# Performance work log

Hardware: AMD Instinct MI355X
Metric: run time of the kernel (lower is better)

## Reference

```python
import jax, jax.numpy as jnp
import numpy as np

LMAX_IN = 3
LMAX_OUT = 3
C = 64          # num_channel
H = 64          # num_channel_hidden
N_NODES = 2048
N_EDGES = 8192

# All coupled (l1, l2, l3) paths with |l1-l2| <= l3 <= min(l1+l2, lmax_out)
COMBS = [(l1, l2, l3)
         for l1 in range(LMAX_IN + 1)
         for l2 in range(LMAX_OUT + 1)
         for l3 in range(abs(l1 - l2), min(l1 + l2, LMAX_OUT) + 1)]
COUNTS = {l3: sum(1 for c in COMBS if c[2] == l3) for l3 in range(LMAX_OUT + 1)}

# Fixed coupling (Clebsch-Gordan-like) tensors for each path, shape (2l1+1, 2l2+1, 2l3+1).
# Deterministic constants (not trained / not differentiated), standing in for the
# e3nn CG coefficients used by InterEinsumTC.
_rng = np.random.RandomState(1234)
CG = [jnp.asarray((_rng.randn(2 * l1 + 1, 2 * l2 + 1, 2 * l3 + 1) * 0.2).astype(np.float32))
      for (l1, l2, l3) in COMBS]


def setup_inputs() -> dict:
    key = jax.random.key(0)
    ks = jax.random.split(key, 16)
    inp = {}
    for l in range(LMAX_OUT + 1):
        inp[f"x{l}"] = jax.random.normal(ks[l], (N_NODES, C, 2 * l + 1), dtype=jnp.float32)
        inp[f"y{l}"] = jax.random.normal(ks[4 + l], (N_EDGES, 2 * l + 1), dtype=jnp.float32)
        fan_in = C * COUNTS[l]
        inp[f"w_lin{l}"] = jax.random.normal(ks[8 + l], (fan_in, H), dtype=jnp.float32) / np.float32(np.sqrt(fan_in))
    inp["ws"] = jax.random.normal(ks[12], (N_EDGES, C * len(COMBS)), dtype=jnp.float32)
    inp["edge_index"] = jax.random.randint(ks[13], (2, N_EDGES), 0, N_NODES, dtype=jnp.int32)
    return inp


def _forward(x0, x1, x2, x3, y0, y1, y2, y3, ws, w_lin0, w_lin1, w_lin2, w_lin3, edge_index):
    xs = (x0, x1, x2, x3)
    ys = (y0, y1, y2, y3)
    wl = (w_lin0, w_lin1, w_lin2, w_lin3)
    src, dst = edge_index[0], edge_index[1]
    # per-edge gather of node features for every input degree
    xg = [x[src] for x in xs]                      # [E, C, 2l1+1]
    buf = {l3: [] for l3 in range(LMAX_OUT + 1)}
    for i, (l1, l2, l3) in enumerate(COMBS):
        # tensor-product contraction: [E, C, 2l3+1]
        out = jnp.einsum('lmn,ecl,em->ecn', CG[i], xg[l1], ys[l2])
        w = ws[:, i * C:(i + 1) * C][:, :, None]   # [E, C, 1] per-path per-channel weight
        buf[l3].append(w * out)
    res = []
    for l3 in range(LMAX_OUT + 1):
        m_ji = jnp.concatenate(buf[l3], axis=1)    # [E, C*count_l3, 2l3+1]
        m_i = jax.ops.segment_sum(m_ji, dst, num_segments=N_NODES)  # scatter-sum -> [N, C*count, 2l3+1]
        res.append(jnp.einsum('ncm,ch->nhm', m_i, wl[l3]))          # per-l3 linear -> [N, H, 2l3+1]
    return tuple(res)


def reference(x0, x1, x2, x3, y0, y1, y2, y3, ws, w_lin0, w_lin1, w_lin2, w_lin3, edge_index):
    return _forward(x0, x1, x2, x3, y0, y1, y2, y3, ws,
                    w_lin0, w_lin1, w_lin2, w_lin3, edge_index)
```

## Files before the change

### kernel.cpp

```cpp
#include <hip/hip_runtime.h>
#include <hip/hip_bf16.h>
#include <cmath>
#include <cstdint>

#define NNODES 2048
#define NEDGES 8192
#define NCH 64
#define NHID 64
#define NPATH 34
#define NTASK (NPATH * NCH)
#define CGTOT 3436
#define MROW 9984
#define TTOT2 888
#define EBLK 8

#define MI_BYTES ((size_t)NNODES * MROW * 2)
#define XT_BYTES ((size_t)NNODES * 16 * NCH * 2)
#define OFF_OFF  (MI_BYTES)
#define CUR_OFF  (OFF_OFF + 2052 * 4)
#define PACK_OFF (CUR_OFF + 2048 * 4)
#define ORD_OFF  (PACK_OFF + 8192 * 4)
#define XT_OFF   (ORD_OFF + 2048 * 4)
#define CGP_OFF  (XT_OFF + XT_BYTES)
#define CGP_FLOATS (TTOT2 * 9)

typedef __attribute__((ext_vector_type(8))) short short8;
typedef __attribute__((ext_vector_type(4))) float floatx4;

struct PathTables {
  int l1[NPATH], l2[NPATH], l3[NPATH];
  int cg_off[NPATH], t_off2[NPATH], rank[NPATH];
  int gpaths[2][20], gnp[2], gbase[2], glen[2];
  int cg_total, ttot2, npaths;
};

constexpr PathTables make_tables() {
  PathTables tb{};
  int np = 0;
  for (int a = 0; a < 4; ++a)
    for (int b = 0; b < 4; ++b) {
      int lo = a > b ? a - b : b - a;
      int hi = a + b < 3 ? a + b : 3;
      for (int c = lo; c <= hi; ++c) { tb.l1[np] = a; tb.l2[np] = b; tb.l3[np] = c; ++np; }
    }
  int cg = 0;
  int cnt[4] = {0, 0, 0, 0};
  for (int i = 0; i < np; ++i) {
    tb.cg_off[i] = cg; tb.rank[i] = cnt[tb.l3[i]]++;
    cg += (2 * tb.l1[i] + 1) * (2 * tb.l2[i] + 1) * (2 * tb.l3[i] + 1);
  }
  int tt2 = 0;
  for (int g = 0; g < 2; ++g) {
    tb.gbase[g] = tt2;
    for (int i = 0; i < np; ++i) {
      int gi = (tb.l3[i] == 0 || tb.l3[i] == 3) ? 0 : 1;
      if (gi != g) continue;
      tb.gpaths[g][tb.gnp[g]++] = i;
      tb.t_off2[i] = tt2;
      int d1 = 2 * tb.l1[i] + 1, d3 = 2 * tb.l3[i] + 1;
      tt2 += ((d1 * d3 + 7) / 8) * 8;
    }
    tb.glen[g] = tt2 - tb.gbase[g];
  }
  tb.cg_total = cg; tb.ttot2 = tt2; tb.npaths = np;
  return tb;
}

constexpr PathTables H_TB = make_tables();
static_assert(H_TB.npaths == NPATH, "npaths");
static_assert(H_TB.cg_total == CGTOT, "cgtot");
static_assert(H_TB.ttot2 == TTOT2, "ttot2");
static_assert(H_TB.gnp[0] == 14 && H_TB.gnp[1] == 20, "gnp");
static_assert(H_TB.gbase[1] == 432 && H_TB.glen[1] == 456, "gsplit");

__constant__ PathTables d_tb = make_tables();

namespace {
struct MT19937 {
  uint32_t mt[624]; int mti; bool has_g; double gval;
  void seed(uint32_t s) {
    for (int i = 0; i < 624; ++i) { mt[i] = s; s = 1812433253u * (s ^ (s >> 30)) + (uint32_t)i + 1u; }
    mti = 624; has_g = false; gval = 0.0;
  }
  uint32_t next() {
    if (mti >= 624) {
      for (int i = 0; i < 624; ++i) {
        uint32_t y = (mt[i] & 0x80000000u) | (mt[(i + 1) % 624] & 0x7fffffffu);
        mt[i] = mt[(i + 397) % 624] ^ (y >> 1) ^ ((y & 1u) ? 0x9908b0dfu : 0u);
      }
      mti = 0;
    }
    uint32_t y = mt[mti++];
    y ^= y >> 11; y ^= (y << 7) & 0x9d2c5680u; y ^= (y << 15) & 0xefc60000u; y ^= y >> 18;
    return y;
  }
  double rdbl() {
    uint32_t a = next() >> 5, b = next() >> 6;
    return ((double)a * 67108864.0 + (double)b) / 9007199254740992.0;
  }
  double gauss() {
    if (has_g) { has_g = false; return gval; }
    double x1, x2, r2;
    do {
      x1 = 2.0 * rdbl() - 1.0;
      x2 = 2.0 * rdbl() - 1.0;
      r2 = x1 * x1 + x2 * x2;
    } while (r2 >= 1.0 || r2 == 0.0);
    double f = std::sqrt(-2.0 * std::log(r2) / r2);
    gval = f * x1; has_g = true;
    return f * x2;
  }
};

float host_pack[CGP_FLOATS];
float* g_cg_dev = nullptr;
bool g_cg_ok = false;

struct CGInit {
  CGInit() {
    static float cg[CGTOT];
    MT19937 g; g.seed(1234u);
    int idx = 0;
    for (int i = 0; i < NPATH; ++i) {
      int d1 = 2 * H_TB.l1[i] + 1, d2 = 2 * H_TB.l2[i] + 1, d3 = 2 * H_TB.l3[i] + 1;
      int sz = d1 * d2 * d3;
      for (int k = 0; k < sz; ++k) cg[idx++] = (float)(g.gauss() * 0.2);
    }
    const int ybase[4] = {0, 1, 4, 9};
    for (int k = 0; k < CGP_FLOATS; ++k) host_pack[k] = 0.f;
    for (int i = 0; i < NPATH; ++i) {
      int d1 = 2 * H_TB.l1[i] + 1, d2 = 2 * H_TB.l2[i] + 1, d3 = 2 * H_TB.l3[i] + 1;
      for (int l = 0; l < d1; ++l)
        for (int n3 = 0; n3 < d3; ++n3) {
          int tt2 = H_TB.t_off2[i] + l * d3 + n3;
          for (int m = 0; m < d2; ++m)
            host_pack[tt2 * 8 + m] = cg[H_TB.cg_off[i] + l * d2 * d3 + m * d3 + n3];
          host_pack[TTOT2 * 8 + tt2] = (float)ybase[H_TB.l2[i]];
        }
    }
    (void)hipHostRegister(host_pack, sizeof(host_pack), hipHostRegisterDefault);
    void* p = nullptr;
    if (hipMalloc(&p, sizeof(host_pack)) == hipSuccess && p) {
      if (hipMemcpy(p, host_pack, sizeof(host_pack), hipMemcpyHostToDevice) == hipSuccess) {
        float back = -1.f;
        if (hipMemcpy(&back, (float*)p + (CGP_FLOATS - 1), sizeof(float),
                      hipMemcpyDeviceToHost) == hipSuccess && back == host_pack[CGP_FLOATS - 1]) {
          g_cg_dev = (float*)p;
          g_cg_ok = true;
        }
      }
    }
  }
} cg_init_instance;
}

__device__ __forceinline__ float bf2f(unsigned short u) {
  union { unsigned int i; float f; } v; v.i = ((unsigned int)u) << 16; return v.f;
}
__device__ __forceinline__ unsigned short f2bf(float f) {
  __hip_bfloat16 h = __float2bfloat16(f);
  union { __hip_bfloat16 h; unsigned short u; } v; v.h = h; return v.u;
}

__global__ __launch_bounds__(1024) void scan_kernel(
    const int* __restrict__ edge_index, int* __restrict__ off, int* __restrict__ cursor,
    int* __restrict__ order)
{
  __shared__ int ldeg[NNODES];
  __shared__ int csum[1024];
  __shared__ int hist[64];
  const int t = threadIdx.x;
  for (int i = t; i < NNODES; i += 1024) ldeg[i] = 0;
  __syncthreads();
  const int* __restrict__ dsts = edge_index + NEDGES;
  for (int e = t; e < NEDGES; e += 1024) atomicAdd(&ldeg[dsts[e]], 1);
  __syncthreads();
  const int l0 = ldeg[2 * t], l1 = ldeg[2 * t + 1];
  const int s = l0 + l1;
  csum[t] = s;
  __syncthreads();
  for (int o = 1; o < 1024; o <<= 1) {
    int v = (t >= o) ? csum[t - o] : 0;
    __syncthreads();
    csum[t] += v;
    __syncthreads();
  }
  int run = csum[t] - s;
  off[2 * t] = run; cursor[2 * t] = run;
  off[2 * t + 1] = run + l0; cursor[2 * t + 1] = run + l0;
  if (t == 0) off[NNODES] = NEDGES;
  if (t < 64) hist[t] = 0;
  __syncthreads();
  for (int i = t; i < NNODES; i += 1024) {
    int d = ldeg[i]; d = d > 63 ? 63 : d;
    atomicAdd(&hist[63 - d], 1);
  }
  __syncthreads();
  if (t == 0) { int r2 = 0; for (int b = 0; b < 64; ++b) { int c = hist[b]; hist[b] = r2; r2 += c; } }
  __syncthreads();
  for (int i = t; i < NNODES; i += 1024) {
    int d = ldeg[i]; d = d > 63 ? 63 : d;
    int pos = atomicAdd(&hist[63 - d], 1);
    order[pos] = i;
  }
}

__global__ __launch_bounds__(256) void fill_xt_kernel(
    const int* __restrict__ edge_index, int* __restrict__ cursor, int* __restrict__ pack,
    const float* __restrict__ x0, const float* __restrict__ x1,
    const float* __restrict__ x2, const float* __restrict__ x3,
    __hip_bfloat16* __restrict__ xT)
{
  const int b = blockIdx.x;
  const int t = threadIdx.x;
  if (b < 32) {
    const int e = b * 256 + t;
    const int d = edge_index[NEDGES + e];
    const int s = edge_index[e];
    const int pos = atomicAdd(&cursor[d], 1);
    pack[pos] = e | (s << 13);
  } else {
    const int n = b - 32;
    for (int idx = t; idx < 1024; idx += 256) {
      const int j = idx >> 6, c = idx & 63;
      const float* src; int d1, m;
      if (j < 1)      { src = x0; d1 = 1; m = j; }
      else if (j < 4) { src = x1; d1 = 3; m = j - 1; }
      else if (j < 9) { src = x2; d1 = 5; m = j - 4; }
      else            { src = x3; d1 = 7; m = j - 9; }
      const float v = src[((size_t)n * NCH + c) * d1 + m];
      xT[((size_t)n * 16 + j) * NCH + c] = __float2bfloat16(v);
    }
  }
}

template <int D1, int D3>
__device__ __forceinline__ void tp_task_run(
    int c, int toff_l, int rank, int nb,
    const float (*Ts)[456], const unsigned short* xs, const float* wv_,
    int n, bool first, __hip_bfloat16* __restrict__ m_out)
{
  constexpr int Kc = (D3 == 1) ? 256 : (D3 == 3) ? 576 : (D3 == 5) ? 704 : 640;
  constexpr int Rc = (D3 == 1) ? 0 : (D3 == 3) ? 256 : (D3 == 5) ? 1984 : 5504;
  constexpr int JB = (D1 == 1) ? 0 : (D1 == 3) ? 1 : (D1 == 5) ? 4 : 9;

  float acc[D3];
#pragma unroll
  for (int m = 0; m < D3; ++m) acc[m] = 0.f;

#pragma unroll
  for (int ei = 0; ei < EBLK; ++ei) {
    if (ei >= nb) break;
    const unsigned short* xr = xs + (ei * 16 + JB) * 64 + c;
    const float* Tp = &Ts[ei][toff_l];
    float u[D3];
#pragma unroll
    for (int m = 0; m < D3; ++m) u[m] = 0.f;
#pragma unroll
    for (int l = 0; l < D1; ++l) {
      const float xv = bf2f(xr[l * 64]);
#pragma unroll
      for (int m = 0; m < D3; ++m) u[m] += xv * Tp[l * D3 + m];
    }
#pragma unroll
    for (int m = 0; m < D3; ++m) acc[m] += wv_[ei] * u[m];
  }

  __hip_bfloat16* mo = m_out + (size_t)n * MROW + Rc + rank * NCH + c;
  if (first) {
#pragma unroll
    for (int m = 0; m < D3; ++m) mo[m * Kc] = __float2bfloat16(acc[m]);
  } else {
#pragma unroll
    for (int m = 0; m < D3; ++m)
      mo[m * Kc] = __float2bfloat16(__bfloat162float(mo[m * Kc]) + acc[m]);
  }
}

__global__ __launch_bounds__(512, 4) void tp_node_kernel(
    const float* __restrict__ y0, const float* __restrict__ y1,
    const float* __restrict__ y2, const float* __restrict__ y3,
    const float* __restrict__ ws, const unsigned short* __restrict__ xT,
    const float* __restrict__ cg_pack,
    const int* __restrict__ off, const int* __restrict__ pack,
    const int* __restrict__ order,
    __hip_bfloat16* __restrict__ m_out)
{
  __shared__ float Ts[EBLK][456];
  __shared__ float y_s[EBLK][18];
  __shared__ int epk[EBLK];
  __shared__ unsigned short xs[EBLK][16][64];

  const int bid = blockIdx.x;
  const int n = order[bid >> 1];
  const int g = bid & 1;
  const int t = threadIdx.x;
  const int beg = off[n];
  const int cnt = off[n + 1] - beg;
  const int gbase = d_tb.gbase[g];
  const int glen  = d_tb.glen[g];
  const int ntask = d_tb.gnp[g] << 6;
  const float* __restrict__ metaf = cg_pack + TTOT2 * 8;

  for (int base = 0; base == 0 || base < cnt; base += EBLK) {
    int nb = cnt - base;
    nb = nb < 0 ? 0 : (nb > EBLK ? EBLK : nb);
    if (t < nb) epk[t] = pack[beg + base + t];
    if (t >= 64 && t < 64 + 2 * EBLK) y_s[(t - 64) >> 1][16 + (t & 1)] = 0.f;
    __syncthreads();
    if (t < nb * 16) {
      const int ei = t >> 4, j = t & 15;
      const int e = epk[ei] & 8191;
      float v;
      if (j < 1)      v = y0[e];
      else if (j < 4) v = y1[e * 3 + (j - 1)];
      else if (j < 9) v = y2[e * 5 + (j - 4)];
      else            v = y3[e * 7 + (j - 9)];
      y_s[ei][j] = v;
    }
    {
      uint2 tmp[4];
      const int tt = t & 255;
      const int eg = (t >> 8) << 2;
#pragma unroll
      for (int e2 = 0; e2 < 4; ++e2) {
        const int ei = eg + e2;
        const int s = (epk[ei] >> 13) & 2047;
        const uint2* __restrict__ src = (const uint2*)(xT + ((size_t)s << 10));
        if (ei < nb) tmp[e2] = src[tt];
      }
#pragma unroll
      for (int e2 = 0; e2 < 4; ++e2) {
        const int ei = eg + e2;
        if (ei < nb) *((uint2*)(&xs[ei][0][0]) + tt) = tmp[e2];
      }
    }
    __syncthreads();
    for (int j = t; j < glen; j += 512) {
      const int tt2 = gbase + j;
      const float4 a = *(const float4*)(cg_pack + tt2 * 8);
      const float4 c4 = *(const float4*)(cg_pack + tt2 * 8 + 4);
      const int yb = (int)metaf[tt2];
      for (int ei = 0; ei < nb; ++ei) {
        const float* yy = &y_s[ei][yb];
        Ts[ei][j] = a.x * yy[0] + a.y * yy[1] + a.z * yy[2] + a.w * yy[3]
                  + c4.x * yy[4] + c4.y * yy[5] + c4.z * yy[6] + c4.w * yy[7];
      }
    }
    __syncthreads();

    const bool first = (base == 0);
    const int c = t & 63;
    float wcur[EBLK], wnxt[EBLK];
    if (t < ntask) {
      const int i0 = d_tb.gpaths[g][t >> 6];
      const int wc0 = (i0 << 6) | (t & 63);
#pragma unroll
      for (int ei = 0; ei < EBLK; ++ei)
        wcur[ei] = (ei < nb) ? ws[(size_t)(epk[ei] & 8191) * NTASK + wc0] : 0.f;
    }
    for (int k = 0; k * 512 + t < ntask; ++k) {
      const int tl = k * 512 + t;
      const int tln = tl + 512;
      const bool more = tln < ntask;
      if (more) {
        const int in = d_tb.gpaths[g][tln >> 6];
        const int wcn = (in << 6) | (tln & 63);
#pragma unroll
        for (int ei = 0; ei < EBLK; ++ei)
          wnxt[ei] = (ei < nb) ? ws[(size_t)(epk[ei] & 8191) * NTASK + wcn] : 0.f;
      }
      const int i = d_tb.gpaths[g][tl >> 6];
      const int toff_l = d_tb.t_off2[i] - gbase;
      const int rk = d_tb.rank[i];
      const int code = d_tb.l1[i] * 4 + d_tb.l3[i];
      switch (code) {
        case  0: tp_task_run<1,1>(c, toff_l, rk, nb, Ts, &xs[0][0][0], wcur, n, first, m_out); break;
        case  1: tp_task_run<1,3>(c, toff_l, rk, nb, Ts, &xs[0][0][0], wcur, n, first, m_out); break;
        case  2: tp_task_run<1,5>(c, toff_l, rk, nb, Ts, &xs[0][0][0], wcur, n, first, m_out); break;
        case  3: tp_task_run<1,7>(c, toff_l, rk, nb, Ts, &xs[0][0][0], wcur, n, first, m_out); break;
        case  4: tp_task_run<3,1>(c, toff_l, rk, nb, Ts, &xs[0][0][0], wcur, n, first, m_out); break;
        case  5: tp_task_run<3,3>(c, toff_l, rk, nb, Ts, &xs[0][0][0], wcur, n, first, m_out); break;
        case  6: tp_task_run<3,5>(c, toff_l, rk, nb, Ts, &xs[0][0][0], wcur, n, first, m_out); break;
        case  7: tp_task_run<3,7>(c, toff_l, rk, nb, Ts, &xs[0][0][0], wcur, n, first, m_out); break;
        case  8: tp_task_run<5,1>(c, toff_l, rk, nb, Ts, &xs[0][0][0], wcur, n, first, m_out); break;
        case  9: tp_task_run<5,3>(c, toff_l, rk, nb, Ts, &xs[0][0][0], wcur, n, first, m_out); break;
        case 10: tp_task_run<5,5>(c, toff_l, rk, nb, Ts, &xs[0][0][0], wcur, n, first, m_out); break;
        case 11: tp_task_run<5,7>(c, toff_l, rk, nb, Ts, &xs[0][0][0], wcur, n, first, m_out); break;
        case 12: tp_task_run<7,1>(c, toff_l, rk, nb, Ts, &xs[0][0][0], wcur, n, first, m_out); break;
        case 13: tp_task_run<7,3>(c, toff_l, rk, nb, Ts, &xs[0][0][0], wcur, n, first, m_out); break;
        case 14: tp_task_run<7,5>(c, toff_l, rk, nb, Ts, &xs[0][0][0], wcur, n, first, m_out); break;
        default: tp_task_run<7,7>(c, toff_l, rk, nb, Ts, &xs[0][0][0], wcur, n, first, m_out); break;
      }
      if (more) {
#pragma unroll
        for (int ei = 0; ei < EBLK; ++ei) wcur[ei] = wnxt[ei];
      }
    }
    __syncthreads();
  }
}

template <int D3, int K, int ROFF>
__device__ __forceinline__ void lin_mfma_body(
    int blk, const unsigned short* __restrict__ mu, const float* __restrict__ wl,
    float* __restrict__ out, unsigned short (*A_s)[72], unsigned short (*W_s)[72])
{
  const int t = threadIdx.x;
  const int wv = t >> 6;
  const int lane = t & 63;
  const int idx16 = lane & 15;
  const int quad = lane >> 4;
  const int r0 = blk * 64;

  floatx4 acc[4] = {{0.f,0.f,0.f,0.f},{0.f,0.f,0.f,0.f},{0.f,0.f,0.f,0.f},{0.f,0.f,0.f,0.f}};

  for (int k0 = 0; k0 < K; k0 += 64) {
    for (int idx = t; idx < 512; idx += 256) {
      const int rr = idx >> 3, ck = (idx & 7) * 8;
      const int r = r0 + rr;
      const int nn = r / D3, mm = r - nn * D3;
      const uint4 v = *(const uint4*)(mu + (size_t)nn * MROW + ROFF + mm * K + k0 + ck);
      *(uint4*)&A_s[rr][ck] = v;
    }
    {
      const int h = t & 63, kg = t >> 6;
      unsigned short tmp[16];
#pragma unroll
      for (int j = 0; j < 16; ++j)
        tmp[j] = f2bf(wl[(size_t)(k0 + kg * 16 + j) * 64 + h]);
      *(uint4*)&W_s[h][kg * 16]     = *(const uint4*)&tmp[0];
      *(uint4*)&W_s[h][kg * 16 + 8] = *(const uint4*)&tmp[8];
    }
    __syncthreads();
#pragma unroll
    for (int ks = 0; ks < 2; ++ks) {
      const int kb = ks * 32 + quad * 8;
      const short8 af = *(const short8*)&A_s[wv * 16 + idx16][kb];
#pragma unroll
      for (int nt = 0; nt < 4; ++nt) {
        const short8 bf = *(const short8*)&W_s[nt * 16 + idx16][kb];
        acc[nt] = __builtin_amdgcn_mfma_f32_16x16x32_bf16(af, bf, acc[nt], 0, 0, 0);
      }
    }
    __syncthreads();
  }

#pragma unroll
  for (int nt = 0; nt < 4; ++nt) {
    const int h = nt * 16 + idx16;
#pragma unroll
    for (int r = 0; r < 4; ++r) {
      const int row = r0 + wv * 16 + quad * 4 + r;
      const int nn = row / D3, mm = row - nn * D3;
      out[((size_t)nn * NHID + h) * D3 + mm] = acc[nt][r];
    }
  }
}

__global__ __launch_bounds__(256) void lin_fused_kernel(
    const unsigned short* __restrict__ mu,
    const float* __restrict__ wl0, const float* __restrict__ wl1,
    const float* __restrict__ wl2, const float* __restrict__ wl3,
    float* __restrict__ out)
{
  __shared__ unsigned short A_s[64][72];
  __shared__ unsigned short W_s[64][72];
  const int b = blockIdx.x;
  if (b < 32)       lin_mfma_body<1, 256, 0>   (b,       mu, wl0, out,           A_s, W_s);
  else if (b < 128) lin_mfma_body<3, 576, 256> (b - 32,  mu, wl1, out + 131072,  A_s, W_s);
  else if (b < 288) lin_mfma_body<5, 704, 1984>(b - 128, mu, wl2, out + 524288,  A_s, W_s);
  else              lin_mfma_body<7, 640, 5504>(b - 288, mu, wl3, out + 1179648, A_s, W_s);
}

extern "C" void kernel_launch(void* const* d_in, const int* in_sizes, int n_in,
                              void* d_out, int out_size, void* d_ws, size_t ws_size,
                              hipStream_t stream) {
  const float* x0  = (const float*)d_in[0];
  const float* y0  = (const float*)d_in[1];
  const float* wl0 = (const float*)d_in[2];
  const float* x1  = (const float*)d_in[3];
  const float* y1  = (const float*)d_in[4];
  const float* wl1 = (const float*)d_in[5];
  const float* x2  = (const float*)d_in[6];
  const float* y2  = (const float*)d_in[7];
  const float* wl2 = (const float*)d_in[8];
  const float* x3  = (const float*)d_in[9];
  const float* y3  = (const float*)d_in[10];
  const float* wl3 = (const float*)d_in[11];
  const float* ws  = (const float*)d_in[12];
  const int* edge_index = (const int*)d_in[13];
  float* out = (float*)d_out;

  __hip_bfloat16* m_i = (__hip_bfloat16*)d_ws;
  int* csr_off = (int*)((char*)d_ws + OFF_OFF);
  int* cursor  = (int*)((char*)d_ws + CUR_OFF);
  int* pack    = (int*)((char*)d_ws + PACK_OFF);
  int* order   = (int*)((char*)d_ws + ORD_OFF);
  __hip_bfloat16* xT = (__hip_bfloat16*)((char*)d_ws + XT_OFF);

  const float* cg_pack;
  if (g_cg_ok) {
    cg_pack = g_cg_dev;
  } else {
    float* cg_ws = (float*)((char*)d_ws + CGP_OFF);
    hipMemcpyAsync(cg_ws, host_pack, sizeof(host_pack), hipMemcpyHostToDevice, stream);
    cg_pack = cg_ws;
  }

  scan_kernel<<<1, 1024, 0, stream>>>(edge_index, csr_off, cursor, order);
  fill_xt_kernel<<<32 + NNODES, 256, 0, stream>>>(edge_index, cursor, pack,
                                                  x0, x1, x2, x3, xT);
  tp_node_kernel<<<2 * NNODES, 512, 0, stream>>>(y0, y1, y2, y3, ws,
                                                 (const unsigned short*)xT, cg_pack,
                                                 csr_off, pack, order, m_i);
  lin_fused_kernel<<<512, 256, 0, stream>>>((const unsigned short*)m_i,
                                            wl0, wl1, wl2, wl3, out);
}
```

Measured before the change: 238.1 us.

## Transpose per-edge CG tables to edge-minor layout and vectorize edge loop

Transposes the shared coupling table from [edge][entry] to [entry][edge] and pads y values into 8-wide aligned slots, so the table build and the tensor-product inner loop can use 128-bit LDS loads across all 8 edges. The inner loop is reordered to iterate over l first, premultiplying edge weights into x and accumulating with fused FMAs. Partial edge blocks are zero-padded, which removes the data-dependent break but always does work for all 8 edges, including empty slots for low-degree nodes.

```diff
diff --git a/kernel.cpp b/kernel.cpp
--- a/kernel.cpp
+++ b/kernel.cpp
@@ -126,7 +126,6 @@
       int sz = d1 * d2 * d3;
       for (int k = 0; k < sz; ++k) cg[idx++] = (float)(g.gauss() * 0.2);
     }
-    const int ybase[4] = {0, 1, 4, 9};
     for (int k = 0; k < CGP_FLOATS; ++k) host_pack[k] = 0.f;
     for (int i = 0; i < NPATH; ++i) {
       int d1 = 2 * H_TB.l1[i] + 1, d2 = 2 * H_TB.l2[i] + 1, d3 = 2 * H_TB.l3[i] + 1;
@@ -135,7 +134,7 @@
           int tt2 = H_TB.t_off2[i] + l * d3 + n3;
           for (int m = 0; m < d2; ++m)
             host_pack[tt2 * 8 + m] = cg[H_TB.cg_off[i] + l * d2 * d3 + m * d3 + n3];
-          host_pack[TTOT2 * 8 + tt2] = (float)ybase[H_TB.l2[i]];
+          host_pack[TTOT2 * 8 + tt2] = (float)H_TB.l2[i];
         }
     }
     (void)hipHostRegister(host_pack, sizeof(host_pack), hipHostRegisterDefault);
@@ -237,33 +236,36 @@
 template <int D1, int D3>
 __device__ __forceinline__ void tp_task_run(
     int c, int toff_l, int rank, int nb,
-    const float (*Ts)[456], const unsigned short* xs, const float* wv_,
+    const float (*Ts)[EBLK], const unsigned short* xs, const float* wv_,
     int n, bool first, __hip_bfloat16* __restrict__ m_out)
 {
   constexpr int Kc = (D3 == 1) ? 256 : (D3 == 3) ? 576 : (D3 == 5) ? 704 : 640;
   constexpr int Rc = (D3 == 1) ? 0 : (D3 == 3) ? 256 : (D3 == 5) ? 1984 : 5504;
   constexpr int JB = (D1 == 1) ? 0 : (D1 == 3) ? 1 : (D1 == 5) ? 4 : 9;
+  (void)nb;
 
   float acc[D3];
 #pragma unroll
   for (int m = 0; m < D3; ++m) acc[m] = 0.f;
 
 #pragma unroll
-  for (int ei = 0; ei < EBLK; ++ei) {
-    if (ei >= nb) break;
-    const unsigned short* xr = xs + (ei * 16 + JB) * 64 + c;
-    const float* Tp = &Ts[ei][toff_l];
-    float u[D3];
-#pragma unroll
-    for (int m = 0; m < D3; ++m) u[m] = 0.f;
-#pragma unroll
-    for (int l = 0; l < D1; ++l) {
-      const float xv = bf2f(xr[l * 64]);
-#pragma unroll
-      for (int m = 0; m < D3; ++m) u[m] += xv * Tp[l * D3 + m];
-    }
-#pragma unroll
-    for (int m = 0; m < D3; ++m) acc[m] += wv_[ei] * u[m];
+  for (int l = 0; l < D1; ++l) {
+    float wx[EBLK];
+#pragma unroll
+    for (int ei = 0; ei < EBLK; ++ei) {
+      const float xv = bf2f(xs[(ei * 16 + JB + l) * 64 + c]);
+      wx[ei] = wv_[ei] * xv;
+    }
+    const float* tr = &Ts[toff_l + l * D3][0];
+#pragma unroll
+    for (int m = 0; m < D3; ++m) {
+      const floatx4 ta = *(const floatx4*)(tr + m * EBLK);
+      const floatx4 tb = *(const floatx4*)(tr + m * EBLK + 4);
+      acc[m] = fmaf(wx[3], ta[3], fmaf(wx[2], ta[2],
+               fmaf(wx[1], ta[1], fmaf(wx[0], ta[0], acc[m]))));
+      acc[m] = fmaf(wx[7], tb[3], fmaf(wx[6], tb[2],
+               fmaf(wx[5], tb[1], fmaf(wx[4], tb[0], acc[m]))));
+    }
   }
 
   __hip_bfloat16* mo = m_out + (size_t)n * MROW + Rc + rank * NCH + c;
@@ -286,8 +288,8 @@
     const int* __restrict__ order,
     __hip_bfloat16* __restrict__ m_out)
 {
-  __shared__ float Ts[EBLK][456];
-  __shared__ float y_s[EBLK][18];
+  __shared__ float Ts[456][EBLK];
+  __shared__ float y_w[EBLK][32];
   __shared__ int epk[EBLK];
   __shared__ unsigned short xs[EBLK][16][64];
 
@@ -305,18 +307,23 @@
   for (int base = 0; base == 0 || base < cnt; base += EBLK) {
     int nb = cnt - base;
     nb = nb < 0 ? 0 : (nb > EBLK ? EBLK : nb);
-    if (t < nb) epk[t] = pack[beg + base + t];
-    if (t >= 64 && t < 64 + 2 * EBLK) y_s[(t - 64) >> 1][16 + (t & 1)] = 0.f;
-    __syncthreads();
-    if (t < nb * 16) {
-      const int ei = t >> 4, j = t & 15;
-      const int e = epk[ei] & 8191;
-      float v;
-      if (j < 1)      v = y0[e];
-      else if (j < 4) v = y1[e * 3 + (j - 1)];
-      else if (j < 9) v = y2[e * 5 + (j - 4)];
-      else            v = y3[e * 7 + (j - 9)];
-      y_s[ei][j] = v;
+    if (t < EBLK) {
+      int pv = 0;
+      if (t < nb) pv = pack[beg + base + t];
+      epk[t] = pv;
+    }
+    __syncthreads();
+    if (t < 256) {
+      const int ei = t >> 5, l2 = (t >> 3) & 3, m8 = t & 7;
+      float v = 0.f;
+      if (ei < nb && m8 < 2 * l2 + 1) {
+        const int e = epk[ei] & 8191;
+        v = (l2 == 0) ? y0[e]
+          : (l2 == 1) ? y1[e * 3 + m8]
+          : (l2 == 2) ? y2[e * 5 + m8]
+          :             y3[e * 7 + m8];
+      }
+      y_w[ei][l2 * 8 + m8] = v;
     }
     {
       uint2 tmp[4];
@@ -327,25 +334,30 @@
         const int ei = eg + e2;
         const int s = (epk[ei] >> 13) & 2047;
         const uint2* __restrict__ src = (const uint2*)(xT + ((size_t)s << 10));
-        if (ei < nb) tmp[e2] = src[tt];
-      }
-#pragma unroll
-      for (int e2 = 0; e2 < 4; ++e2) {
-        const int ei = eg + e2;
-        if (ei < nb) *((uint2*)(&xs[ei][0][0]) + tt) = tmp[e2];
-      }
+        uint2 z; z.x = 0u; z.y = 0u;
+        tmp[e2] = (ei < nb) ? src[tt] : z;
+      }
+#pragma unroll
+      for (int e2 = 0; e2 < 4; ++e2)
+        *((uint2*)(&xs[eg + e2][0][0]) + tt) = tmp[e2];
     }
     __syncthreads();
     for (int j = t; j < glen; j += 512) {
       const int tt2 = gbase + j;
-      const float4 a = *(const float4*)(cg_pack + tt2 * 8);
+      const float4 a  = *(const float4*)(cg_pack + tt2 * 8);
       const float4 c4 = *(const float4*)(cg_pack + tt2 * 8 + 4);
-      const int yb = (int)metaf[tt2];
-      for (int ei = 0; ei < nb; ++ei) {
-        const float* yy = &y_s[ei][yb];
-        Ts[ei][j] = a.x * yy[0] + a.y * yy[1] + a.z * yy[2] + a.w * yy[3]
-                  + c4.x * yy[4] + c4.y * yy[5] + c4.z * yy[6] + c4.w * yy[7];
-      }
+      const int l2i = (int)metaf[tt2];
+      float tv[EBLK];
+#pragma unroll
+      for (int ei = 0; ei < EBLK; ++ei) {
+        const float* yy = &y_w[ei][l2i * 8];
+        const float4 ya = *(const float4*)yy;
+        const float4 yb = *(const float4*)(yy + 4);
+        tv[ei] = a.x * ya.x + a.y * ya.y + a.z * ya.z + a.w * ya.w
+               + c4.x * yb.x + c4.y * yb.y + c4.z * yb.z + c4.w * yb.w;
+      }
+      *(float4*)&Ts[j][0] = make_float4(tv[0], tv[1], tv[2], tv[3]);
+      *(float4*)&Ts[j][4] = make_float4(tv[4], tv[5], tv[6], tv[7]);
     }
     __syncthreads();
 
```

Measured after the change: 262.2 us. 1.1x slower.
